# Optimization experiments

Measured on AMD Instinct MI355X. Metric: run time of the kernel, lower is better.

## Reference

```python
import jax, jax.numpy as jnp
import numpy as np

COUPLING = 0.12
EPS = 1e-08
EMBED_DIM = 16
H = 4
REL_MAX_DIST = 64
PAST_LEN = 524288


def setup_inputs() -> dict:
    key = jax.random.key(0)
    ks = jax.random.split(key, 7)
    return {
        "candidate": jax.random.normal(ks[0], (EMBED_DIM, 2), dtype=jnp.float32),
        "z_past": jax.random.normal(ks[1], (PAST_LEN, EMBED_DIM, 2), dtype=jnp.float32),
        "heads_w": jax.random.normal(ks[2], (H, 2 * EMBED_DIM, 4 * EMBED_DIM), dtype=jnp.float32) * 0.05,
        "heads_b": jax.random.normal(ks[3], (H, 2 * EMBED_DIM), dtype=jnp.float32) * 0.05,
        "out_w": jax.random.normal(ks[4], (2 * EMBED_DIM, H * 2 * EMBED_DIM), dtype=jnp.float32) * 0.05,
        "out_b": jax.random.normal(ks[5], (2 * EMBED_DIM,), dtype=jnp.float32) * 0.05,
        "rel_bias": jax.random.normal(ks[6], (2 * REL_MAX_DIST + 1, 2), dtype=jnp.float32) * 0.02,
        "norm_scale": jnp.ones((1,), dtype=jnp.float32),
        "pos": PAST_LEN,
    }


def reference(candidate, z_past, heads_w, heads_b, out_w, out_b, rel_bias, norm_scale, pos):
    # candidate: [D,2] (real/imag), z_past: [P,D,2]
    P, D = z_past.shape[0], z_past.shape[1]
    # features_c = cat([z_curr_rep, z_past], -1); view_as_real + flatten -> [P, 4D]
    feats = jnp.concatenate(
        [jnp.broadcast_to(candidate[None], (P, D, 2)), z_past], axis=1
    ).reshape(P, 4 * D)
    # 4 small MLP heads, tanh, concat: [P, H, 2D] -> mean over past -> [H*2D]
    h = jnp.tanh(jnp.einsum("pd,hod->pho", feats, heads_w) + heads_b[None])
    combined_mean = h.reshape(P, -1).mean(axis=0)
    out = out_w @ combined_mean + out_b          # [2D]
    mod = out.reshape(D, 2)                      # complex mod as real/imag pair
    # relative positional bias: mean over gathered (clipped) indices
    rel = jnp.arange(pos - P, pos)
    idx = jnp.clip(rel + REL_MAX_DIST, 0, 2 * REL_MAX_DIST)
    bias_mean = rel_bias[idx].mean(axis=0)       # [2]
    # z_new = candidate + COUPLING * (mod + bias_mean)
    z = candidate + COUPLING * (mod + bias_mean[None, :])
    # tanh applied independently to real and imag parts
    z = jnp.tanh(z)
    max_int = jnp.max(jnp.sum(z * z, axis=-1))   # max |z|^2
    scale = norm_scale[0] / jnp.sqrt(max_int + EPS)
    return jnp.where(max_int > 0, z * scale, z)  # [D,2]
```

## Files before the change

### kernel.cpp

```cpp
#include <hip/hip_runtime.h>
#include <hip/hip_bf16.h>
#include <math.h>

#define COUPLING 0.12f
#define EPSV 1e-8f
#define SCALE2L2E 2.8853900817779268f

typedef __attribute__((ext_vector_type(8))) short bf16x8;
typedef __attribute__((ext_vector_type(4))) float f32x4;

__device__ __forceinline__ float tanh_from_e2(float y) {
    float e = __builtin_amdgcn_exp2f(y);
    float r = __builtin_amdgcn_rcpf(1.0f + e);
    return fmaf(-2.0f, r, 1.0f);
}
__device__ __forceinline__ float tanh_fast(float x) {
    return tanh_from_e2(SCALE2L2E * x);
}
__device__ __forceinline__ float sig_e2(float y) {
    float e = __builtin_amdgcn_exp2f(y);
    return __builtin_amdgcn_rcpf(1.0f + e);
}

__device__ __forceinline__ short f2bf(float f) {
    __hip_bfloat16 h = __float2bfloat16(f);
    return __builtin_bit_cast(short, h);
}

__global__ __launch_bounds__(256, 4) void phot_main(
    const float* __restrict__ z_past,
    const float* __restrict__ heads_w,
    const float* __restrict__ heads_b,
    const float* __restrict__ cand,
    float* __restrict__ partials,
    int P, int NB)
{
    __shared__ float wacc[128];
    __shared__ float cpre_l[128];
    __shared__ __align__(16) unsigned short zb[3][4][512];

    const int tid  = threadIdx.x;
    const int lane = tid & 63;
    const int wv   = tid >> 6;
    const int col  = lane & 15;
    const int kg   = lane >> 4;

    if (tid < 128) {
        const float* wr = heads_w + (size_t)tid * 64;
        float s0 = heads_b[tid], s1 = 0.f, s2 = 0.f, s3 = 0.f;
        #pragma unroll
        for (int k = 0; k < 32; k += 4) {
            s0 = fmaf(wr[k+0], cand[k+0], s0);
            s1 = fmaf(wr[k+1], cand[k+1], s1);
            s2 = fmaf(wr[k+2], cand[k+2], s2);
            s3 = fmaf(wr[k+3], cand[k+3], s3);
        }
        cpre_l[tid] = SCALE2L2E * ((s0 + s1) + (s2 + s3));
    }

    const int g0 = wv * 2, g1 = g0 + 1;
    bf16x8 bfA, bfB;
    {
        const float* wA = heads_w + (size_t)(g0 * 16 + col) * 64 + 32 + kg * 8;
        const float* wB = heads_w + (size_t)(g1 * 16 + col) * 64 + 32 + kg * 8;
        f32x4 a0 = *(const f32x4*)wA, a1 = *(const f32x4*)(wA + 4);
        f32x4 b0 = *(const f32x4*)wB, b1 = *(const f32x4*)(wB + 4);
        bfA[0]=f2bf(SCALE2L2E*a0[0]); bfA[1]=f2bf(SCALE2L2E*a0[1]);
        bfA[2]=f2bf(SCALE2L2E*a0[2]); bfA[3]=f2bf(SCALE2L2E*a0[3]);
        bfA[4]=f2bf(SCALE2L2E*a1[0]); bfA[5]=f2bf(SCALE2L2E*a1[1]);
        bfA[6]=f2bf(SCALE2L2E*a1[2]); bfA[7]=f2bf(SCALE2L2E*a1[3]);
        bfB[0]=f2bf(SCALE2L2E*b0[0]); bfB[1]=f2bf(SCALE2L2E*b0[1]);
        bfB[2]=f2bf(SCALE2L2E*b0[2]); bfB[3]=f2bf(SCALE2L2E*b0[3]);
        bfB[4]=f2bf(SCALE2L2E*b1[0]); bfB[5]=f2bf(SCALE2L2E*b1[1]);
        bfB[6]=f2bf(SCALE2L2E*b1[2]); bfB[7]=f2bf(SCALE2L2E*b1[3]);
    }
    __syncthreads();
    const float cpA = cpre_l[g0 * 16 + col];
    const float cpB = cpre_l[g1 * 16 + col];
    const f32x4 cvA = {cpA, cpA, cpA, cpA};
    const f32x4 cvB = {cpB, cpB, cpB, cpB};

    f32x4 accA = {0,0,0,0}, accB = {0,0,0,0};

    const int T  = (P + 15) >> 4;
    const int Tf = P >> 4;
    const int b  = blockIdx.x;
    const int K  = (b < T) ? ((T - 1 - b) / NB + 1) : 0;
    const int PH = (K + 3) >> 2;

    const bool uni = ((T % NB) == 0) && (Tf == T) && ((K & 7) == 0);

    const int sr = lane >> 2;
    const int sc = lane & 3;
    const int woff = sr * 32 + ((sc ^ ((sr >> 1) & 3)) << 3);
    const int roff = col * 32 + ((kg ^ ((col >> 1) & 3)) << 3);

    f32x4 preA0, preB0, preA1, preB1;

    #define SLOADP(ph, S) { \
        const int j_ = 4 * (ph) + wv; \
        if (j_ < K) { \
            const int tt_ = b + j_ * NB; \
            int grow = tt_ * 16 + sr; if (grow > P - 1) grow = P - 1; \
            const float* g_ = z_past + (size_t)grow * 32 + sc * 8; \
            preA##S = *(const f32x4*)g_; \
            preB##S = *(const f32x4*)(g_ + 4); \
        } }
    #define SWRITEP(ph, S) { \
        const int j_ = 4 * (ph) + wv; \
        if (j_ < K) { \
            bf16x8 w_; \
            w_[0]=f2bf(preA##S[0]); w_[1]=f2bf(preA##S[1]); \
            w_[2]=f2bf(preA##S[2]); w_[3]=f2bf(preA##S[3]); \
            w_[4]=f2bf(preB##S[0]); w_[5]=f2bf(preB##S[1]); \
            w_[6]=f2bf(preB##S[2]); w_[7]=f2bf(preB##S[3]); \
            *(bf16x8*)(&zb[(ph) % 3][wv][woff]) = w_; \
        } }
    #define CTILE_F(p, j) { \
        const bf16x8 a_ = *(const bf16x8*)(&zb[(p) % 3][j][roff]); \
        f32x4 d_ = __builtin_amdgcn_mfma_f32_16x16x32_bf16(a_, bfA, cvA, 0, 0, 0); \
        accA[0] += sig_e2(d_[0]); accA[1] += sig_e2(d_[1]); \
        accA[2] += sig_e2(d_[2]); accA[3] += sig_e2(d_[3]); \
        d_ = __builtin_amdgcn_mfma_f32_16x16x32_bf16(a_, bfB, cvB, 0, 0, 0); \
        accB[0] += sig_e2(d_[0]); accB[1] += sig_e2(d_[1]); \
        accB[2] += sig_e2(d_[2]); accB[3] += sig_e2(d_[3]); }
    #define CTILE_G(p, j) { \
        const int jj_ = 4 * (p) + (j); \
        if (jj_ < K) { \
            const int tt_ = b + jj_ * NB; \
            const bf16x8 a_ = *(const bf16x8*)(&zb[(p) % 3][j][roff]); \
            const int base_ = tt_ * 16; \
            if (base_ + 16 <= P) { \
                f32x4 d_ = __builtin_amdgcn_mfma_f32_16x16x32_bf16(a_, bfA, cvA, 0, 0, 0); \
                accA[0] += sig_e2(d_[0]); accA[1] += sig_e2(d_[1]); \
                accA[2] += sig_e2(d_[2]); accA[3] += sig_e2(d_[3]); \
                d_ = __builtin_amdgcn_mfma_f32_16x16x32_bf16(a_, bfB, cvB, 0, 0, 0); \
                accB[0] += sig_e2(d_[0]); accB[1] += sig_e2(d_[1]); \
                accB[2] += sig_e2(d_[2]); accB[3] += sig_e2(d_[3]); \
            } else { \
                const int r0_ = base_ + kg * 4; \
                f32x4 d_ = __builtin_amdgcn_mfma_f32_16x16x32_bf16(a_, bfA, cvA, 0, 0, 0); \
                if (r0_ + 0 < P) accA[0] += sig_e2(d_[0]); \
                if (r0_ + 1 < P) accA[1] += sig_e2(d_[1]); \
                if (r0_ + 2 < P) accA[2] += sig_e2(d_[2]); \
                if (r0_ + 3 < P) accA[3] += sig_e2(d_[3]); \
                d_ = __builtin_amdgcn_mfma_f32_16x16x32_bf16(a_, bfB, cvB, 0, 0, 0); \
                if (r0_ + 0 < P) accB[0] += sig_e2(d_[0]); \
                if (r0_ + 1 < P) accB[1] += sig_e2(d_[1]); \
                if (r0_ + 2 < P) accB[2] += sig_e2(d_[2]); \
                if (r0_ + 3 < P) accB[3] += sig_e2(d_[3]); \
            } \
        } }

    #define SYNC { asm volatile("s_waitcnt lgkmcnt(0)" ::: "memory"); \
                   __builtin_amdgcn_s_barrier(); \
                   __builtin_amdgcn_sched_barrier(0); }

    if (K > 0) {
        SLOADP(0, 0)
        SWRITEP(0, 0)
        SLOADP(1, 1)
        SYNC

        if (uni) {
            for (int p = 0; p < PH; p += 2) {
                {
                    SLOADP(p + 2, 0)
                    CTILE_F(p, 0) CTILE_F(p, 1) CTILE_F(p, 2) CTILE_F(p, 3)
                    SWRITEP(p + 1, 1)
                    SYNC
                }
                {
                    SLOADP(p + 3, 1)
                    CTILE_F(p + 1, 0) CTILE_F(p + 1, 1) CTILE_F(p + 1, 2) CTILE_F(p + 1, 3)
                    SWRITEP(p + 2, 0)
                    SYNC
                }
            }
        } else {
            for (int p = 0; p < PH; p += 2) {
                {
                    SLOADP(p + 2, 0)
                    CTILE_G(p, 0) CTILE_G(p, 1) CTILE_G(p, 2) CTILE_G(p, 3)
                    SWRITEP(p + 1, 1)
                    SYNC
                }
                if (p + 1 < PH) {
                    SLOADP(p + 3, 1)
                    CTILE_G(p + 1, 0) CTILE_G(p + 1, 1) CTILE_G(p + 1, 2) CTILE_G(p + 1, 3)
                    SWRITEP(p + 2, 0)
                    SYNC
                }
            }
        }
    }
    #undef SLOADP
    #undef SWRITEP
    #undef CTILE_F
    #undef CTILE_G
    #undef SYNC

    float nsum = 0.0f;
    if (K > 0) {
        int nfull = (b < Tf) ? ((Tf - 1 - b) / NB + 1) : 0;
        nsum = 4.0f * (float)nfull;
        if (Tf < T && b <= Tf && ((Tf - b) % NB) == 0) {
            int prem = P - Tf * 16;
            int nv = prem - kg * 4; if (nv < 0) nv = 0; if (nv > 4) nv = 4;
            nsum += (float)nv;
        }
    }

    float sA = nsum - 2.0f * ((accA[0] + accA[1]) + (accA[2] + accA[3]));
    sA += __shfl_xor(sA, 16, 64);
    sA += __shfl_xor(sA, 32, 64);
    float sB = nsum - 2.0f * ((accB[0] + accB[1]) + (accB[2] + accB[3]));
    sB += __shfl_xor(sB, 16, 64);
    sB += __shfl_xor(sB, 32, 64);
    if (lane < 16) {
        wacc[g0 * 16 + lane] = sA;
        wacc[g1 * 16 + lane] = sB;
    }
    __syncthreads();
    if (tid < 128) {
        partials[(size_t)b * 128 + tid] = wacc[tid];
    }
}

__global__ __launch_bounds__(1024) void phot_finalize(
    const float* __restrict__ partials, int nblk, int P,
    const float* __restrict__ out_w,
    const float* __restrict__ out_b,
    const float* __restrict__ rel_bias,
    const float* __restrict__ cand,
    const float* __restrict__ norm_scale,
    const int* __restrict__ posp,
    float* __restrict__ out)
{
    __shared__ __align__(16) float sh[4096];
    __shared__ float  cm[128];
    __shared__ float  outv[32];
    __shared__ double db[512];
    __shared__ float  bm[2];

    const int t   = threadIdx.x;
    const int chg = t & 31;
    const int sl  = t >> 5;

    const int cnt = nblk >> 5;
    const float* p0 = partials + (size_t)(sl * cnt) * 128 + chg * 4;
    f32x4 s0 = {0,0,0,0}, s1 = {0,0,0,0}, s2 = {0,0,0,0}, s3 = {0,0,0,0};
    int i = 0;
    for (; i + 16 <= cnt; i += 16) {
        f32x4 v[16];
        #pragma unroll
        for (int j = 0; j < 16; ++j)
            v[j] = *(const f32x4*)(p0 + (size_t)(i + j) * 128);
        #pragma unroll
        for (int j = 0; j < 16; j += 4) {
            s0 += v[j+0]; s1 += v[j+1]; s2 += v[j+2]; s3 += v[j+3];
        }
    }
    for (; i < cnt; ++i) s0 += *(const f32x4*)(p0 + (size_t)i * 128);
    f32x4 acc = (s0 + s1) + (s2 + s3);
    *(f32x4*)&sh[sl * 128 + chg * 4] = acc;
    __syncthreads();

    if (t < 128) {
        float s = 0.0f;
        #pragma unroll
        for (int s2i = 0; s2i < 32; ++s2i) s += sh[t + 128 * s2i];
        cm[t] = s / (float)P;
    }

    if (t < 512) {
        const int c = t >> 8, j = t & 255;
        double v = 0.0;
        if (j <= 128) {
            const long long pos = (long long)(*posp);
            const long long a = pos - (long long)P + 64;
            double cnt2;
            if (j == 0) {
                long long hi = -a; if (hi > (long long)P - 1) hi = (long long)P - 1;
                cnt2 = (hi >= 0) ? (double)(hi + 1) : 0.0;
            } else if (j == 128) {
                long long lo = 128 - a; if (lo < 0) lo = 0;
                cnt2 = (lo <= (long long)P - 1) ? (double)((long long)P - lo) : 0.0;
            } else {
                long long p = (long long)j - a;
                cnt2 = (p >= 0 && p < (long long)P) ? 1.0 : 0.0;
            }
            v = cnt2 * (double)rel_bias[2*j + c];
        }
        db[t] = v;
    }
    __syncthreads();
    #pragma unroll
    for (int s = 128; s >= 1; s >>= 1) {
        if (t < 512 && (t & 255) < s) db[t] += db[t + s];
        __syncthreads();
    }
    if (t < 2) bm[t] = (float)(db[t << 8] / (double)P);
    __syncthreads();

    if (t < 32) {
        const float* wr = out_w + t * 128;
        float o0 = out_b[t], o1 = 0.f, o2 = 0.f, o3 = 0.f;
        #pragma unroll
        for (int j = 0; j < 128; j += 4) {
            o0 = fmaf(wr[j+0], cm[j+0], o0);
            o1 = fmaf(wr[j+1], cm[j+1], o1);
            o2 = fmaf(wr[j+2], cm[j+2], o2);
            o3 = fmaf(wr[j+3], cm[j+3], o3);
        }
        outv[t] = (o0+o1) + (o2+o3);
    }
    __syncthreads();

    if (t < 32) {
        float zt = tanh_fast(cand[t] + COUPLING * (outv[t] + bm[t & 1]));
        float other = __shfl_xor(zt, 1, 64);
        float m = fmaf(zt, zt, other * other);
        #pragma unroll
        for (int off = 2; off < 32; off <<= 1) m = fmaxf(m, __shfl_xor(m, off, 64));
        float scale = norm_scale[0] / sqrtf(m + EPSV);
        out[t] = (m > 0.0f) ? zt * scale : zt;
    }
}

extern "C" void kernel_launch(void* const* d_in, const int* in_sizes, int n_in,
                              void* d_out, int out_size, void* d_ws, size_t ws_size,
                              hipStream_t stream)
{
    const float* cand       = (const float*)d_in[0];
    const float* z_past     = (const float*)d_in[1];
    const float* heads_w    = (const float*)d_in[2];
    const float* heads_b    = (const float*)d_in[3];
    const float* out_w      = (const float*)d_in[4];
    const float* out_b      = (const float*)d_in[5];
    const float* rel_bias   = (const float*)d_in[6];
    const float* norm_scale = (const float*)d_in[7];
    const int*   posp       = (const int*)d_in[8];

    const int P = in_sizes[1] / 32;

    int nblk = 2048;
    size_t need = (size_t)nblk * 128 * sizeof(float);
    if (need > ws_size) {
        nblk = (int)(ws_size / (128 * sizeof(float)));
        nblk &= ~31;
        if (nblk < 32) nblk = 32;
    }
    float* partials = (float*)d_ws;

    phot_main<<<nblk, 256, 0, stream>>>(z_past, heads_w, heads_b, cand,
                                        partials, P, nblk);
    phot_finalize<<<1, 1024, 0, stream>>>(partials, nblk, P, out_w, out_b,
                                          rel_bias, cand, norm_scale, posp,
                                          (float*)d_out);
}
```

Measured before the change: 43.84 us.

## Replace LDS-staged tile pipeline with direct per-wave global loads into MFMA operands

Drops the triple-buffered shared-memory staging of z_past tiles and the block-wide barriers. Each wave now loads its 16x32 tile straight from global memory into the MFMA A-operand layout, with one-tile-ahead register prefetch. The goal is to remove the LDS write/read round trips and the barrier stalls. In exchange, the four waves of a block each issue loads for the same tile, relying on cache hits, and prefetch depth is shallower.

```diff
diff --git a/kernel.cpp b/kernel.cpp
--- a/kernel.cpp
+++ b/kernel.cpp
@@ -37,7 +37,6 @@
 {
     __shared__ float wacc[128];
     __shared__ float cpre_l[128];
-    __shared__ __align__(16) unsigned short zb[3][4][512];
 
     const int tid  = threadIdx.x;
     const int lane = tid & 63;
@@ -86,119 +85,68 @@
     const int Tf = P >> 4;
     const int b  = blockIdx.x;
     const int K  = (b < T) ? ((T - 1 - b) / NB + 1) : 0;
-    const int PH = (K + 3) >> 2;
-
-    const bool uni = ((T % NB) == 0) && (Tf == T) && ((K & 7) == 0);
-
-    const int sr = lane >> 2;
-    const int sc = lane & 3;
-    const int woff = sr * 32 + ((sc ^ ((sr >> 1) & 3)) << 3);
-    const int roff = col * 32 + ((kg ^ ((col >> 1) & 3)) << 3);
-
-    f32x4 preA0, preB0, preA1, preB1;
-
-    #define SLOADP(ph, S) { \
-        const int j_ = 4 * (ph) + wv; \
-        if (j_ < K) { \
-            const int tt_ = b + j_ * NB; \
-            int grow = tt_ * 16 + sr; if (grow > P - 1) grow = P - 1; \
-            const float* g_ = z_past + (size_t)grow * 32 + sc * 8; \
-            preA##S = *(const f32x4*)g_; \
-            preB##S = *(const f32x4*)(g_ + 4); \
-        } }
-    #define SWRITEP(ph, S) { \
-        const int j_ = 4 * (ph) + wv; \
-        if (j_ < K) { \
-            bf16x8 w_; \
-            w_[0]=f2bf(preA##S[0]); w_[1]=f2bf(preA##S[1]); \
-            w_[2]=f2bf(preA##S[2]); w_[3]=f2bf(preA##S[3]); \
-            w_[4]=f2bf(preB##S[0]); w_[5]=f2bf(preB##S[1]); \
-            w_[6]=f2bf(preB##S[2]); w_[7]=f2bf(preB##S[3]); \
-            *(bf16x8*)(&zb[(ph) % 3][wv][woff]) = w_; \
-        } }
-    #define CTILE_F(p, j) { \
-        const bf16x8 a_ = *(const bf16x8*)(&zb[(p) % 3][j][roff]); \
-        f32x4 d_ = __builtin_amdgcn_mfma_f32_16x16x32_bf16(a_, bfA, cvA, 0, 0, 0); \
-        accA[0] += sig_e2(d_[0]); accA[1] += sig_e2(d_[1]); \
-        accA[2] += sig_e2(d_[2]); accA[3] += sig_e2(d_[3]); \
-        d_ = __builtin_amdgcn_mfma_f32_16x16x32_bf16(a_, bfB, cvB, 0, 0, 0); \
-        accB[0] += sig_e2(d_[0]); accB[1] += sig_e2(d_[1]); \
-        accB[2] += sig_e2(d_[2]); accB[3] += sig_e2(d_[3]); }
-    #define CTILE_G(p, j) { \
-        const int jj_ = 4 * (p) + (j); \
-        if (jj_ < K) { \
-            const int tt_ = b + jj_ * NB; \
-            const bf16x8 a_ = *(const bf16x8*)(&zb[(p) % 3][j][roff]); \
-            const int base_ = tt_ * 16; \
-            if (base_ + 16 <= P) { \
-                f32x4 d_ = __builtin_amdgcn_mfma_f32_16x16x32_bf16(a_, bfA, cvA, 0, 0, 0); \
-                accA[0] += sig_e2(d_[0]); accA[1] += sig_e2(d_[1]); \
-                accA[2] += sig_e2(d_[2]); accA[3] += sig_e2(d_[3]); \
-                d_ = __builtin_amdgcn_mfma_f32_16x16x32_bf16(a_, bfB, cvB, 0, 0, 0); \
-                accB[0] += sig_e2(d_[0]); accB[1] += sig_e2(d_[1]); \
-                accB[2] += sig_e2(d_[2]); accB[3] += sig_e2(d_[3]); \
-            } else { \
-                const int r0_ = base_ + kg * 4; \
-                f32x4 d_ = __builtin_amdgcn_mfma_f32_16x16x32_bf16(a_, bfA, cvA, 0, 0, 0); \
-                if (r0_ + 0 < P) accA[0] += sig_e2(d_[0]); \
-                if (r0_ + 1 < P) accA[1] += sig_e2(d_[1]); \
-                if (r0_ + 2 < P) accA[2] += sig_e2(d_[2]); \
-                if (r0_ + 3 < P) accA[3] += sig_e2(d_[3]); \
-                d_ = __builtin_amdgcn_mfma_f32_16x16x32_bf16(a_, bfB, cvB, 0, 0, 0); \
-                if (r0_ + 0 < P) accB[0] += sig_e2(d_[0]); \
-                if (r0_ + 1 < P) accB[1] += sig_e2(d_[1]); \
-                if (r0_ + 2 < P) accB[2] += sig_e2(d_[2]); \
-                if (r0_ + 3 < P) accB[3] += sig_e2(d_[3]); \
-            } \
-        } }
-
-    #define SYNC { asm volatile("s_waitcnt lgkmcnt(0)" ::: "memory"); \
-                   __builtin_amdgcn_s_barrier(); \
-                   __builtin_amdgcn_sched_barrier(0); }
+
+    const bool uni = ((T % NB) == 0) && (Tf == T);
 
     if (K > 0) {
-        SLOADP(0, 0)
-        SWRITEP(0, 0)
-        SLOADP(1, 1)
-        SYNC
-
         if (uni) {
-            for (int p = 0; p < PH; p += 2) {
-                {
-                    SLOADP(p + 2, 0)
-                    CTILE_F(p, 0) CTILE_F(p, 1) CTILE_F(p, 2) CTILE_F(p, 3)
-                    SWRITEP(p + 1, 1)
-                    SYNC
+            int row = b * 16 + col;
+            const float* g = z_past + (size_t)row * 32 + kg * 8;
+            f32x4 cl = *(const f32x4*)g;
+            f32x4 ch = *(const f32x4*)(g + 4);
+            const size_t step = (size_t)NB * 16 * 32;
+            for (int k = 0; k < K; ++k) {
+                f32x4 nl, nh;
+                if (k + 1 < K) {
+                    const float* gn = g + (size_t)(k + 1) * step;
+                    nl = *(const f32x4*)gn;
+                    nh = *(const f32x4*)(gn + 4);
                 }
-                {
-                    SLOADP(p + 3, 1)
-                    CTILE_F(p + 1, 0) CTILE_F(p + 1, 1) CTILE_F(p + 1, 2) CTILE_F(p + 1, 3)
-                    SWRITEP(p + 2, 0)
-                    SYNC
+                bf16x8 a;
+                a[0]=f2bf(cl[0]); a[1]=f2bf(cl[1]); a[2]=f2bf(cl[2]); a[3]=f2bf(cl[3]);
+                a[4]=f2bf(ch[0]); a[5]=f2bf(ch[1]); a[6]=f2bf(ch[2]); a[7]=f2bf(ch[3]);
+                f32x4 d = __builtin_amdgcn_mfma_f32_16x16x32_bf16(a, bfA, cvA, 0, 0, 0);
+                accA[0] += sig_e2(d[0]); accA[1] += sig_e2(d[1]);
+                accA[2] += sig_e2(d[2]); accA[3] += sig_e2(d[3]);
+                d = __builtin_amdgcn_mfma_f32_16x16x32_bf16(a, bfB, cvB, 0, 0, 0);
+                accB[0] += sig_e2(d[0]); accB[1] += sig_e2(d[1]);
+                accB[2] += sig_e2(d[2]); accB[3] += sig_e2(d[3]);
+                cl = nl; ch = nh;
+            }
+        } else {
+            for (int k = 0; k < K; ++k) {
+                const int t = b + k * NB;
+                int row = t * 16 + col; if (row > P - 1) row = P - 1;
+                const float* g = z_past + (size_t)row * 32 + kg * 8;
+                f32x4 cl = *(const f32x4*)g;
+                f32x4 ch = *(const f32x4*)(g + 4);
+                bf16x8 a;
+                a[0]=f2bf(cl[0]); a[1]=f2bf(cl[1]); a[2]=f2bf(cl[2]); a[3]=f2bf(cl[3]);
+                a[4]=f2bf(ch[0]); a[5]=f2bf(ch[1]); a[6]=f2bf(ch[2]); a[7]=f2bf(ch[3]);
+                const int base = t * 16;
+                if (base + 16 <= P) {
+                    f32x4 d = __builtin_amdgcn_mfma_f32_16x16x32_bf16(a, bfA, cvA, 0, 0, 0);
+                    accA[0] += sig_e2(d[0]); accA[1] += sig_e2(d[1]);
+                    accA[2] += sig_e2(d[2]); accA[3] += sig_e2(d[3]);
+                    d = __builtin_amdgcn_mfma_f32_16x16x32_bf16(a, bfB, cvB, 0, 0, 0);
+                    accB[0] += sig_e2(d[0]); accB[1] += sig_e2(d[1]);
+                    accB[2] += sig_e2(d[2]); accB[3] += sig_e2(d[3]);
+                } else {
+                    const int r0 = base + kg * 4;
+                    f32x4 d = __builtin_amdgcn_mfma_f32_16x16x32_bf16(a, bfA, cvA, 0, 0, 0);
+                    if (r0 + 0 < P) accA[0] += sig_e2(d[0]);
+                    if (r0 + 1 < P) accA[1] += sig_e2(d[1]);
+                    if (r0 + 2 < P) accA[2] += sig_e2(d[2]);
+                    if (r0 + 3 < P) accA[3] += sig_e2(d[3]);
+                    d = __builtin_amdgcn_mfma_f32_16x16x32_bf16(a, bfB, cvB, 0, 0, 0);
+                    if (r0 + 0 < P) accB[0] += sig_e2(d[0]);
+                    if (r0 + 1 < P) accB[1] += sig_e2(d[1]);
+                    if (r0 + 2 < P) accB[2] += sig_e2(d[2]);
+                    if (r0 + 3 < P) accB[3] += sig_e2(d[3]);
                 }
             }
-        } else {
-            for (int p = 0; p < PH; p += 2) {
-                {
-                    SLOADP(p + 2, 0)
-                    CTILE_G(p, 0) CTILE_G(p, 1) CTILE_G(p, 2) CTILE_G(p, 3)
-                    SWRITEP(p + 1, 1)
-                    SYNC
-                }
-                if (p + 1 < PH) {
-                    SLOADP(p + 3, 1)
-                    CTILE_G(p + 1, 0) CTILE_G(p + 1, 1) CTILE_G(p + 1, 2) CTILE_G(p + 1, 3)
-                    SWRITEP(p + 2, 0)
-                    SYNC
-                }
-            }
-        }
-    }
-    #undef SLOADP
-    #undef SWRITEP
-    #undef CTILE_F
-    #undef CTILE_G
-    #undef SYNC
+        }
+    }
 
     float nsum = 0.0f;
     if (K > 0) {
```

Result: slower. 56.20 us (+28.2%).
